# Optimization experiments

Measured on AMD Instinct MI355X. Metric: run time of the kernel, lower is better.

Reference implementation:

```python
import math
import jax, jax.numpy as jnp
import numpy as np

B, N, C = 16, 2048, 128
ETA, TAU = 1.0, 1.5


def setup_inputs() -> dict:
    key = jax.random.key(0)
    k1, k2, k3, k4, k5 = jax.random.split(key, 5)
    H_t = jax.random.normal(k1, (B, N, C), dtype=jnp.float32)
    A_stat = jax.random.uniform(k2, (N, N), dtype=jnp.float32)
    M_mask = jax.random.uniform(k3, (N, N), dtype=jnp.float32)
    # nn.Linear(d_model, d_model, bias=False) weights, shape [out, in]
    scale = 1.0 / math.sqrt(C)
    Wq = jax.random.uniform(k4, (C, C), dtype=jnp.float32, minval=-scale, maxval=scale)
    Wk = jax.random.uniform(k5, (C, C), dtype=jnp.float32, minval=-scale, maxval=scale)
    return {"H_t": H_t, "A_stat": A_stat, "M_mask": M_mask, "Wq": Wq, "Wk": Wk}


def reference(H_t, A_stat, M_mask, Wq, Wk):
    c = H_t.shape[-1]
    neg_inf = jnp.array(-jnp.inf, dtype=H_t.dtype)
    # Linear: x @ W.T
    Q = jnp.einsum('bnc,dc->bnd', H_t, Wq)
    K = jnp.einsum('bnc,dc->bnd', H_t, Wk)
    # scaled QK^T, temperature
    logits = jnp.einsum('bnd,bmd->bnm', Q, K) / (math.sqrt(c) * TAU)
    # symmetrize
    logits = 0.5 * (logits + jnp.swapaxes(logits, -1, -2))
    # diagonal mask
    n = logits.shape[-1]
    eye = jnp.eye(n, dtype=bool)
    logits = jnp.where(eye[None, :, :], neg_inf, logits)
    # static-adjacency bias with zeroed diagonal
    A_bias = jnp.where(eye, 0.0, A_stat)
    logits = logits + ETA * A_bias[None, :, :]
    # external mask
    logits = jnp.where((M_mask <= 0)[None, :, :], neg_inf, logits)
    return jax.nn.softmax(logits, axis=-1)
```

## Files before the change

### kernel.cpp

```cpp
#include <hip/hip_runtime.h>
#include <hip/hip_bf16.h>
#include <hip/hip_fp16.h>
#include <math.h>

#define Bn 16
#define Nn 2048
#define Cn 128

typedef __attribute__((ext_vector_type(8))) short bf16x8;
typedef __attribute__((ext_vector_type(4))) float f32x4;

constexpr float SCALE = 0.029462782549439476f;
constexpr float SHIFT = 4.0f;

#define LDS_STRIDE 136

__device__ __forceinline__ const bf16x8* as_frag(const __hip_bfloat16* p){
    return reinterpret_cast<const bf16x8*>(p);
}

__global__ __launch_bounds__(256) void prep_kernel(
    const float* __restrict__ A, const float* __restrict__ M, __half* __restrict__ CB,
    const float* __restrict__ Wq, const float* __restrict__ Wk,
    float* __restrict__ WqT, float* __restrict__ WkT)
{
    size_t idx = (size_t)blockIdx.x * 256 + threadIdx.x;
    int n = (int)(idx >> 11), m = (int)(idx & (Nn-1));
    float a = A[idx];
    float mm = M[idx];
    float v = (mm <= 0.0f || n == m) ? -INFINITY : a;
    CB[idx] = __float2half(v);
    if (blockIdx.x < 64) {
        int widx = (int)idx;
        int d = widx >> 7, c = widx & 127;
        WqT[c*Cn + d] = Wq[widx];
        WkT[c*Cn + d] = Wk[widx];
    }
}

__global__ __launch_bounds__(256) void qk_kernel(
    const float* __restrict__ H, const float* __restrict__ WqT, const float* __restrict__ WkT,
    __hip_bfloat16* __restrict__ Qb, __hip_bfloat16* __restrict__ Kb)
{
    __shared__ __align__(16) float Hs[32*Cn];
    const int t = threadIdx.x;
    const size_t row0 = (size_t)blockIdx.x * 32;
    const float4* src = reinterpret_cast<const float4*>(H + row0*Cn);
    float4* dst = reinterpret_cast<float4*>(Hs);
    #pragma unroll
    for (int i = 0; i < 4; i++) dst[i*256 + t] = src[i*256 + t];
    __syncthreads();
    const int d = t & 127, rh = t >> 7;
    float accq[16], acck[16];
    #pragma unroll
    for (int r = 0; r < 16; r++){ accq[r] = 0.f; acck[r] = 0.f; }
    for (int cb = 0; cb < Cn; cb += 4){
        float wq[4], wk[4];
        #pragma unroll
        for (int j = 0; j < 4; j++){ wq[j] = WqT[(cb+j)*Cn + d]; wk[j] = WkT[(cb+j)*Cn + d]; }
        #pragma unroll
        for (int r = 0; r < 16; r++){
            float4 h = *reinterpret_cast<const float4*>(&Hs[(rh*16+r)*Cn + cb]);
            accq[r] += h.x*wq[0] + h.y*wq[1] + h.z*wq[2] + h.w*wq[3];
            acck[r] += h.x*wk[0] + h.y*wk[1] + h.z*wk[2] + h.w*wk[3];
        }
    }
    #pragma unroll
    for (int r = 0; r < 16; r++){
        size_t row = row0 + rh*16 + r;
        Qb[row*Cn + d] = __float2bfloat16(accq[r]);
        Kb[row*Cn + d] = __float2bfloat16(acck[r]);
    }
}

__global__ __launch_bounds__(256) void attn_e_kernel(
    const __hip_bfloat16* __restrict__ Qb, const __hip_bfloat16* __restrict__ Kb,
    const __half* __restrict__ CB, float* __restrict__ rowsum, float* __restrict__ out)
{
    __shared__ __align__(16) __hip_bfloat16 Ks_s[64*LDS_STRIDE];
    __shared__ __align__(16) __hip_bfloat16 Qs_s[64*LDS_STRIDE];
    const int t = threadIdx.x;
    const int wave = t >> 6, lane = t & 63;
    const int q = lane >> 4, lc = lane & 15;
    const int batch = blockIdx.y;
    const int n0 = blockIdx.x * 64;
    const size_t rbase = (size_t)batch * Nn;

    const int nA = n0 + wave*16 + lc;
    bf16x8 aQ[4], aK[4];
    #pragma unroll
    for (int ks = 0; ks < 4; ks++){
        aQ[ks] = *as_frag(Qb + (rbase + nA)*Cn + ks*32 + q*8);
        aK[ks] = *as_frag(Kb + (rbase + nA)*Cn + ks*32 + q*8);
    }

    int nout[4];
    #pragma unroll
    for (int r = 0; r < 4; r++) nout[r] = n0 + wave*16 + q*4 + r;

    float sumacc[4] = {0.f,0.f,0.f,0.f};

    for (int mc = 0; mc < Nn/64; mc++){
        __syncthreads();
        {
            const int4* gK = reinterpret_cast<const int4*>(Kb + (rbase + (size_t)mc*64)*Cn);
            const int4* gQ = reinterpret_cast<const int4*>(Qb + (rbase + (size_t)mc*64)*Cn);
            #pragma unroll
            for (int i = 0; i < 4; i++){
                int id = i*256 + t;
                int r = id >> 4, c2 = id & 15;
                int4 vk = gK[id];
                int4 vq = gQ[id];
                *reinterpret_cast<int4*>(&Ks_s[r*LDS_STRIDE + c2*8]) = vk;
                *reinterpret_cast<int4*>(&Qs_s[r*LDS_STRIDE + c2*8]) = vq;
            }
        }
        __syncthreads();
        #pragma unroll
        for (int mt = 0; mt < 4; mt++){
            const int m0 = mc*64 + mt*16;
            bf16x8 bK[4], bQ[4];
            #pragma unroll
            for (int ks = 0; ks < 4; ks++){
                bK[ks] = *as_frag(&Ks_s[(mt*16+lc)*LDS_STRIDE + ks*32 + q*8]);
                bQ[ks] = *as_frag(&Qs_s[(mt*16+lc)*LDS_STRIDE + ks*32 + q*8]);
            }
            f32x4 acc = {0.f,0.f,0.f,0.f};
            #pragma unroll
            for (int ks = 0; ks < 4; ks++){
                acc = __builtin_amdgcn_mfma_f32_16x16x32_bf16(aQ[ks], bK[ks], acc, 0, 0, 0);
                acc = __builtin_amdgcn_mfma_f32_16x16x32_bf16(aK[ks], bQ[ks], acc, 0, 0, 0);
            }
            const int m = m0 + lc;
            #pragma unroll
            for (int r = 0; r < 4; r++){
                const int n = nout[r];
                float logit = fmaf(acc[r], SCALE, __half2float(CB[(size_t)n*Nn + m]));
                float e = __expf(logit - SHIFT);
                sumacc[r] += e;
                out[(rbase + n)*Nn + m] = e;
            }
        }
    }
    #pragma unroll
    for (int r = 0; r < 4; r++){
        float s = sumacc[r];
        s += __shfl_xor(s, 1);
        s += __shfl_xor(s, 2);
        s += __shfl_xor(s, 4);
        s += __shfl_xor(s, 8);
        if (lc == 0) rowsum[rbase + nout[r]] = 1.0f / s;
    }
}

__global__ __launch_bounds__(256) void norm_kernel(
    float* __restrict__ out, const float* __restrict__ rsinv)
{
    const size_t t0 = (size_t)blockIdx.x * 256 + threadIdx.x;
    const size_t stride = (size_t)4096 * 256;
    float4* o4 = reinterpret_cast<float4*>(out);
    #pragma unroll
    for (int i = 0; i < 16; i++){
        size_t idx = t0 + (size_t)i * stride;
        float4 v = o4[idx];
        float r = rsinv[idx >> 9];
        v.x *= r; v.y *= r; v.z *= r; v.w *= r;
        o4[idx] = v;
    }
}

extern "C" void kernel_launch(void* const* d_in, const int* in_sizes, int n_in,
                              void* d_out, int out_size, void* d_ws, size_t ws_size,
                              hipStream_t stream)
{
    const float* H  = (const float*)d_in[0];
    const float* A  = (const float*)d_in[1];
    const float* M  = (const float*)d_in[2];
    const float* Wq = (const float*)d_in[3];
    const float* Wk = (const float*)d_in[4];
    float* out = (float*)d_out;
    char* ws = (char*)d_ws;
    __hip_bfloat16* Qb = (__hip_bfloat16*)(ws + 0);
    __hip_bfloat16* Kb = (__hip_bfloat16*)(ws + 8388608);
    float* rowsum      = (float*)(ws + 16777216);
    float* WqT         = (float*)(ws + 16908288);
    float* WkT         = (float*)(ws + 16973824);
    __half* CB         = (__half*)(ws + 17039360);

    prep_kernel<<<(Nn*Nn)/256, 256, 0, stream>>>(A, M, CB, Wq, Wk, WqT, WkT);
    qk_kernel<<<(Bn*Nn)/32, 256, 0, stream>>>(H, WqT, WkT, Qb, Kb);
    attn_e_kernel<<<dim3(Nn/64, Bn), 256, 0, stream>>>(Qb, Kb, CB, rowsum, out);
    norm_kernel<<<4096, 256, 0, stream>>>(out, rowsum);
}
```

Measured before the change: 510.9 us.

## Replace write-then-normalize with two-pass rowsum and recompute attention kernels

```diff
diff --git a/kernel.cpp b/kernel.cpp
--- a/kernel.cpp
+++ b/kernel.cpp
@@ -13,10 +13,15 @@
 constexpr float SCALE = 0.029462782549439476f;
 constexpr float SHIFT = 4.0f;
 
-#define LDS_STRIDE 136
-
-__device__ __forceinline__ const bf16x8* as_frag(const __hip_bfloat16* p){
+__device__ __forceinline__ const bf16x8* as_frag(const void* p){
     return reinterpret_cast<const bf16x8*>(p);
+}
+
+__device__ __forceinline__ void load16_lds(const void* g, void* l){
+    __builtin_amdgcn_global_load_lds(
+        (const __attribute__((address_space(1))) void*)g,
+        (__attribute__((address_space(3))) void*)l,
+        16, 0, 0);
 }
 
 __global__ __launch_bounds__(256) void prep_kernel(
@@ -73,46 +78,74 @@
     }
 }
 
-__global__ __launch_bounds__(256) void attn_e_kernel(
+template<int PASS>
+__global__ __launch_bounds__(256) void attn_kernel(
     const __hip_bfloat16* __restrict__ Qb, const __hip_bfloat16* __restrict__ Kb,
     const __half* __restrict__ CB, float* __restrict__ rowsum, float* __restrict__ out)
 {
-    __shared__ __align__(16) __hip_bfloat16 Ks_s[64*LDS_STRIDE];
-    __shared__ __align__(16) __hip_bfloat16 Qs_s[64*LDS_STRIDE];
+    __shared__ __align__(16) char Ks_s[64*256];
+    __shared__ __align__(16) char Qs_s[64*256];
     const int t = threadIdx.x;
     const int wave = t >> 6, lane = t & 63;
     const int q = lane >> 4, lc = lane & 15;
+    const int rb = blockIdx.x & 15, ch = blockIdx.x >> 4;
     const int batch = blockIdx.y;
-    const int n0 = blockIdx.x * 64;
+    const int n0 = rb * 128;
     const size_t rbase = (size_t)batch * Nn;
 
-    const int nA = n0 + wave*16 + lc;
-    bf16x8 aQ[4], aK[4];
-    #pragma unroll
-    for (int ks = 0; ks < 4; ks++){
-        aQ[ks] = *as_frag(Qb + (rbase + nA)*Cn + ks*32 + q*8);
-        aK[ks] = *as_frag(Kb + (rbase + nA)*Cn + ks*32 + q*8);
-    }
-
-    int nout[4];
-    #pragma unroll
-    for (int r = 0; r < 4; r++) nout[r] = n0 + wave*16 + q*4 + r;
-
-    float sumacc[4] = {0.f,0.f,0.f,0.f};
-
-    for (int mc = 0; mc < Nn/64; mc++){
+    bf16x8 aQ[2][4], aK[2][4];
+    #pragma unroll
+    for (int g = 0; g < 2; g++){
+        const int nA = n0 + wave*32 + g*16 + lc;
+        #pragma unroll
+        for (int ks = 0; ks < 4; ks++){
+            aQ[g][ks] = *as_frag(Qb + (rbase + nA)*Cn + ks*32 + q*8);
+            aK[g][ks] = *as_frag(Kb + (rbase + nA)*Cn + ks*32 + q*8);
+        }
+    }
+
+    int nout[2][4];
+    #pragma unroll
+    for (int g = 0; g < 2; g++)
+        #pragma unroll
+        for (int r = 0; r < 4; r++) nout[g][r] = n0 + wave*32 + g*16 + q*4 + r;
+
+    float rs_inv[2][4];
+    if (PASS == 1){
+        #pragma unroll
+        for (int g = 0; g < 2; g++)
+            #pragma unroll
+            for (int r = 0; r < 4; r++){
+                float s = rowsum[rbase + nout[g][r]] + rowsum[(size_t)Bn*Nn + rbase + nout[g][r]];
+                rs_inv[g][r] = 1.0f / s;
+            }
+    }
+
+    float sumacc[2][4] = {{0.f,0.f,0.f,0.f},{0.f,0.f,0.f,0.f}};
+
+    const int laneoffE = ((lane >> 4) << 8) + ((((lane & 15) ^ (lane >> 4))) << 4);
+    int coff[4];
+    #pragma unroll
+    for (int ks = 0; ks < 4; ks++) coff[ks] = (((4*ks + q) ^ (lc & 7)) << 4);
+    const int rowoff = lc * 256;
+
+    const char* gkb = (const char*)Kb;
+    const char* gqb = (const char*)Qb;
+    const char* gt0 = (wave < 2) ? gkb : gqb;
+    void* lt = (wave < 2) ? (void*)Ks_s : (void*)Qs_s;
+    const int idx0 = (wave & 1) * 8;
+
+    const int mc0 = ch * (Nn/128);
+    for (int mc = mc0; mc < mc0 + Nn/128; mc++){
         __syncthreads();
         {
-            const int4* gK = reinterpret_cast<const int4*>(Kb + (rbase + (size_t)mc*64)*Cn);
-            const int4* gQ = reinterpret_cast<const int4*>(Qb + (rbase + (size_t)mc*64)*Cn);
-            #pragma unroll
-            for (int i = 0; i < 4; i++){
-                int id = i*256 + t;
-                int r = id >> 4, c2 = id & 15;
-                int4 vk = gK[id];
-                int4 vq = gQ[id];
-                *reinterpret_cast<int4*>(&Ks_s[r*LDS_STRIDE + c2*8]) = vk;
-                *reinterpret_cast<int4*>(&Qs_s[r*LDS_STRIDE + c2*8]) = vq;
+            const size_t tileoff = (rbase + (size_t)mc*64) * (Cn*2);
+            const char* gt = gt0 + tileoff;
+            #pragma unroll
+            for (int j = 0; j < 8; j++){
+                const int idx = idx0 + j;
+                const int lo = laneoffE ^ ((j & 1) << 6);
+                load16_lds(gt + idx*1024 + lo, (char*)lt + idx*1024);
             }
         }
         __syncthreads();
@@ -122,50 +155,42 @@
             bf16x8 bK[4], bQ[4];
             #pragma unroll
             for (int ks = 0; ks < 4; ks++){
-                bK[ks] = *as_frag(&Ks_s[(mt*16+lc)*LDS_STRIDE + ks*32 + q*8]);
-                bQ[ks] = *as_frag(&Qs_s[(mt*16+lc)*LDS_STRIDE + ks*32 + q*8]);
-            }
-            f32x4 acc = {0.f,0.f,0.f,0.f};
-            #pragma unroll
-            for (int ks = 0; ks < 4; ks++){
-                acc = __builtin_amdgcn_mfma_f32_16x16x32_bf16(aQ[ks], bK[ks], acc, 0, 0, 0);
-                acc = __builtin_amdgcn_mfma_f32_16x16x32_bf16(aK[ks], bQ[ks], acc, 0, 0, 0);
+                bK[ks] = *as_frag(Ks_s + mt*4096 + rowoff + coff[ks]);
+                bQ[ks] = *as_frag(Qs_s + mt*4096 + rowoff + coff[ks]);
             }
             const int m = m0 + lc;
             #pragma unroll
+            for (int g = 0; g < 2; g++){
+                f32x4 acc = {0.f,0.f,0.f,0.f};
+                #pragma unroll
+                for (int ks = 0; ks < 4; ks++){
+                    acc = __builtin_amdgcn_mfma_f32_16x16x32_bf16(aQ[g][ks], bK[ks], acc, 0, 0, 0);
+                    acc = __builtin_amdgcn_mfma_f32_16x16x32_bf16(aK[g][ks], bQ[ks], acc, 0, 0, 0);
+                }
+                #pragma unroll
+                for (int r = 0; r < 4; r++){
+                    const int n = nout[g][r];
+                    float logit = fmaf(acc[r], SCALE, __half2float(CB[(size_t)n*Nn + m]));
+                    float e = __expf(logit - SHIFT);
+                    if (PASS == 0) sumacc[g][r] += e;
+                    else out[(rbase + n)*Nn + m] = e * rs_inv[g][r];
+                }
+            }
+        }
+    }
+    if (PASS == 0){
+        float* rs = rowsum + (size_t)ch * (Bn*Nn);
+        #pragma unroll
+        for (int g = 0; g < 2; g++)
+            #pragma unroll
             for (int r = 0; r < 4; r++){
-                const int n = nout[r];
-                float logit = fmaf(acc[r], SCALE, __half2float(CB[(size_t)n*Nn + m]));
-                float e = __expf(logit - SHIFT);
-                sumacc[r] += e;
-                out[(rbase + n)*Nn + m] = e;
-            }
-        }
-    }
-    #pragma unroll
-    for (int r = 0; r < 4; r++){
-        float s = sumacc[r];
-        s += __shfl_xor(s, 1);
-        s += __shfl_xor(s, 2);
-        s += __shfl_xor(s, 4);
-        s += __shfl_xor(s, 8);
-        if (lc == 0) rowsum[rbase + nout[r]] = 1.0f / s;
-    }
-}
-
-__global__ __launch_bounds__(256) void norm_kernel(
-    float* __restrict__ out, const float* __restrict__ rsinv)
-{
-    const size_t t0 = (size_t)blockIdx.x * 256 + threadIdx.x;
-    const size_t stride = (size_t)4096 * 256;
-    float4* o4 = reinterpret_cast<float4*>(out);
-    #pragma unroll
-    for (int i = 0; i < 16; i++){
-        size_t idx = t0 + (size_t)i * stride;
-        float4 v = o4[idx];
-        float r = rsinv[idx >> 9];
-        v.x *= r; v.y *= r; v.z *= r; v.w *= r;
-        o4[idx] = v;
+                float s = sumacc[g][r];
+                s += __shfl_xor(s, 1);
+                s += __shfl_xor(s, 2);
+                s += __shfl_xor(s, 4);
+                s += __shfl_xor(s, 8);
+                if (lc == 0) rs[rbase + nout[g][r]] = s;
+            }
     }
 }
 
@@ -183,12 +208,12 @@
     __hip_bfloat16* Qb = (__hip_bfloat16*)(ws + 0);
     __hip_bfloat16* Kb = (__hip_bfloat16*)(ws + 8388608);
     float* rowsum      = (float*)(ws + 16777216);
-    float* WqT         = (float*)(ws + 16908288);
-    float* WkT         = (float*)(ws + 16973824);
-    __half* CB         = (__half*)(ws + 17039360);
+    float* WqT         = (float*)(ws + 17825792);
+    float* WkT         = (float*)(ws + 17891328);
+    __half* CB         = (__half*)(ws + 17956864);
 
     prep_kernel<<<(Nn*Nn)/256, 256, 0, stream>>>(A, M, CB, Wq, Wk, WqT, WkT);
     qk_kernel<<<(Bn*Nn)/32, 256, 0, stream>>>(H, WqT, WkT, Qb, Kb);
-    attn_e_kernel<<<dim3(Nn/64, Bn), 256, 0, stream>>>(Qb, Kb, CB, rowsum, out);
-    norm_kernel<<<4096, 256, 0, stream>>>(out, rowsum);
-}
+    attn_kernel<0><<<dim3(32, Bn), 256, 0, stream>>>(Qb, Kb, CB, rowsum, out);
+    attn_kernel<1><<<dim3(32, Bn), 256, 0, stream>>>(Qb, Kb, CB, rowsum, out);
+}
```

Result: faster. 455.6 us (-10.8%).

## Fuse softmax normalization into attention kernel, holding fp16 exps in registers

Applied to the files above, without the earlier changes.

```diff
diff --git a/kernel.cpp b/kernel.cpp
--- a/kernel.cpp
+++ b/kernel.cpp
@@ -13,10 +13,15 @@
 constexpr float SCALE = 0.029462782549439476f;
 constexpr float SHIFT = 4.0f;
 
-#define LDS_STRIDE 136
-
-__device__ __forceinline__ const bf16x8* as_frag(const __hip_bfloat16* p){
+__device__ __forceinline__ const bf16x8* as_frag(const void* p){
     return reinterpret_cast<const bf16x8*>(p);
+}
+
+__device__ __forceinline__ void load16_lds(const void* g, void* l){
+    __builtin_amdgcn_global_load_lds(
+        (const __attribute__((address_space(1))) void*)g,
+        (__attribute__((address_space(3))) void*)l,
+        16, 0, 0);
 }
 
 __global__ __launch_bounds__(256) void prep_kernel(
@@ -73,20 +78,26 @@
     }
 }
 
-__global__ __launch_bounds__(256) void attn_e_kernel(
+__global__ __launch_bounds__(512, 2) void attn_onepass_kernel(
     const __hip_bfloat16* __restrict__ Qb, const __hip_bfloat16* __restrict__ Kb,
-    const __half* __restrict__ CB, float* __restrict__ rowsum, float* __restrict__ out)
-{
-    __shared__ __align__(16) __hip_bfloat16 Ks_s[64*LDS_STRIDE];
-    __shared__ __align__(16) __hip_bfloat16 Qs_s[64*LDS_STRIDE];
+    const __half* __restrict__ CB, float* __restrict__ out)
+{
+    __shared__ __align__(16) char tiles[4][2][16384];
+    __shared__ float psum[4][32];
     const int t = threadIdx.x;
     const int wave = t >> 6, lane = t & 63;
     const int q = lane >> 4, lc = lane & 15;
-    const int batch = blockIdx.y;
-    const int n0 = blockIdx.x * 64;
-    const size_t rbase = (size_t)batch * Nn;
-
-    const int nA = n0 + wave*16 + lc;
+    const int qt = wave >> 1;
+    const int rg = wave & 1;
+
+    const int h = blockIdx.x;
+    const int logical = (h & 7) * 128 + (h >> 3);
+    const int bx = logical & 63;
+    const int by = logical >> 6;
+    const int n0 = bx * 32;
+    const size_t rbase = (size_t)by * Nn;
+
+    const int nA = n0 + rg*16 + lc;
     bf16x8 aQ[4], aK[4];
     #pragma unroll
     for (int ks = 0; ks < 4; ks++){
@@ -96,34 +107,39 @@
 
     int nout[4];
     #pragma unroll
-    for (int r = 0; r < 4; r++) nout[r] = n0 + wave*16 + q*4 + r;
-
+    for (int r = 0; r < 4; r++) nout[r] = n0 + rg*16 + q*4 + r;
+
+    const int laneoffE = ((lane >> 4) << 8) + ((((lane & 15) ^ (lane >> 4))) << 4);
+    int coff[4];
+    #pragma unroll
+    for (int ks = 0; ks < 4; ks++) coff[ks] = (((4*ks + q) ^ (lc & 7)) << 4);
+    const int rowoff = lc * 256;
+
+    const char* gsrc0 = rg ? (const char*)Qb : (const char*)Kb;
+    char* ldst = tiles[qt][rg];
+
+    unsigned int ep[4][16];
     float sumacc[4] = {0.f,0.f,0.f,0.f};
 
-    for (int mc = 0; mc < Nn/64; mc++){
+    #pragma unroll
+    for (int mc = 0; mc < 8; mc++){
         __syncthreads();
-        {
-            const int4* gK = reinterpret_cast<const int4*>(Kb + (rbase + (size_t)mc*64)*Cn);
-            const int4* gQ = reinterpret_cast<const int4*>(Qb + (rbase + (size_t)mc*64)*Cn);
-            #pragma unroll
-            for (int i = 0; i < 4; i++){
-                int id = i*256 + t;
-                int r = id >> 4, c2 = id & 15;
-                int4 vk = gK[id];
-                int4 vq = gQ[id];
-                *reinterpret_cast<int4*>(&Ks_s[r*LDS_STRIDE + c2*8]) = vk;
-                *reinterpret_cast<int4*>(&Qs_s[r*LDS_STRIDE + c2*8]) = vq;
-            }
+        const size_t tileoff = (rbase + (size_t)qt*512 + (size_t)mc*64) * (Cn*2);
+        const char* gt = gsrc0 + tileoff;
+        #pragma unroll
+        for (int idx = 0; idx < 16; idx++){
+            const int lo = laneoffE ^ ((idx & 1) << 6);
+            load16_lds(gt + idx*1024 + lo, ldst + idx*1024);
         }
         __syncthreads();
         #pragma unroll
         for (int mt = 0; mt < 4; mt++){
-            const int m0 = mc*64 + mt*16;
+            const int mtg = mc*4 + mt;
             bf16x8 bK[4], bQ[4];
             #pragma unroll
             for (int ks = 0; ks < 4; ks++){
-                bK[ks] = *as_frag(&Ks_s[(mt*16+lc)*LDS_STRIDE + ks*32 + q*8]);
-                bQ[ks] = *as_frag(&Qs_s[(mt*16+lc)*LDS_STRIDE + ks*32 + q*8]);
+                bK[ks] = *as_frag(tiles[qt][0] + mt*4096 + rowoff + coff[ks]);
+                bQ[ks] = *as_frag(tiles[qt][1] + mt*4096 + rowoff + coff[ks]);
             }
             f32x4 acc = {0.f,0.f,0.f,0.f};
             #pragma unroll
@@ -131,17 +147,19 @@
                 acc = __builtin_amdgcn_mfma_f32_16x16x32_bf16(aQ[ks], bK[ks], acc, 0, 0, 0);
                 acc = __builtin_amdgcn_mfma_f32_16x16x32_bf16(aK[ks], bQ[ks], acc, 0, 0, 0);
             }
-            const int m = m0 + lc;
+            const int m = qt*512 + mtg*16 + lc;
             #pragma unroll
             for (int r = 0; r < 4; r++){
-                const int n = nout[r];
-                float logit = fmaf(acc[r], SCALE, __half2float(CB[(size_t)n*Nn + m]));
+                float logit = fmaf(acc[r], SCALE, __half2float(CB[(size_t)nout[r]*Nn + m]));
                 float e = __expf(logit - SHIFT);
                 sumacc[r] += e;
-                out[(rbase + n)*Nn + m] = e;
+                unsigned int he = (unsigned int)__half_as_ushort(__float2half(e));
+                if ((mtg & 1) == 0) ep[r][mtg>>1] = he;
+                else                ep[r][mtg>>1] |= (he << 16);
             }
         }
     }
+
     #pragma unroll
     for (int r = 0; r < 4; r++){
         float s = sumacc[r];
@@ -149,23 +167,27 @@
         s += __shfl_xor(s, 2);
         s += __shfl_xor(s, 4);
         s += __shfl_xor(s, 8);
-        if (lc == 0) rowsum[rbase + nout[r]] = 1.0f / s;
-    }
-}
-
-__global__ __launch_bounds__(256) void norm_kernel(
-    float* __restrict__ out, const float* __restrict__ rsinv)
-{
-    const size_t t0 = (size_t)blockIdx.x * 256 + threadIdx.x;
-    const size_t stride = (size_t)4096 * 256;
-    float4* o4 = reinterpret_cast<float4*>(out);
-    #pragma unroll
-    for (int i = 0; i < 16; i++){
-        size_t idx = t0 + (size_t)i * stride;
-        float4 v = o4[idx];
-        float r = rsinv[idx >> 9];
-        v.x *= r; v.y *= r; v.z *= r; v.w *= r;
-        o4[idx] = v;
+        if (lc == 0) psum[qt][rg*16 + q*4 + r] = s;
+    }
+    __syncthreads();
+    float rs[4];
+    #pragma unroll
+    for (int r = 0; r < 4; r++){
+        const int rl = rg*16 + q*4 + r;
+        rs[r] = 1.0f / (psum[0][rl] + psum[1][rl] + psum[2][rl] + psum[3][rl]);
+    }
+
+    #pragma unroll
+    for (int r = 0; r < 4; r++){
+        float* orow = out + (rbase + nout[r])*Nn + qt*512 + lc;
+        #pragma unroll
+        for (int k = 0; k < 16; k++){
+            const unsigned int p = ep[r][k];
+            const float elo = __half2float(__ushort_as_half((unsigned short)(p & 0xFFFFu)));
+            const float ehi = __half2float(__ushort_as_half((unsigned short)(p >> 16)));
+            orow[(2*k)*16]   = elo * rs[r];
+            orow[(2*k+1)*16] = ehi * rs[r];
+        }
     }
 }
 
@@ -182,13 +204,11 @@
     char* ws = (char*)d_ws;
     __hip_bfloat16* Qb = (__hip_bfloat16*)(ws + 0);
     __hip_bfloat16* Kb = (__hip_bfloat16*)(ws + 8388608);
-    float* rowsum      = (float*)(ws + 16777216);
-    float* WqT         = (float*)(ws + 16908288);
-    float* WkT         = (float*)(ws + 16973824);
-    __half* CB         = (__half*)(ws + 17039360);
+    float* WqT         = (float*)(ws + 16777216);
+    float* WkT         = (float*)(ws + 16842752);
+    __half* CB         = (__half*)(ws + 16908288);
 
     prep_kernel<<<(Nn*Nn)/256, 256, 0, stream>>>(A, M, CB, Wq, Wk, WqT, WkT);
     qk_kernel<<<(Bn*Nn)/32, 256, 0, stream>>>(H, WqT, WkT, Qb, Kb);
-    attn_e_kernel<<<dim3(Nn/64, Bn), 256, 0, stream>>>(Qb, Kb, CB, rowsum, out);
-    norm_kernel<<<4096, 256, 0, stream>>>(out, rowsum);
-}
+    attn_onepass_kernel<<<dim3((Nn/32) * Bn), 512, 0, stream>>>(Qb, Kb, CB, out);
+}
```

Result: faster. 439.2 us (-14.0%).
